# Kernel optimization log

Measured on AMD Instinct MI355X. Metric: run time of the kernel, lower is better.

The kernel has to match this reference:

```python
import jax, jax.numpy as jnp
import numpy as np

KERNEL_MUL = 2.0
KERNEL_NUM = 5


def _mmd(source, target):
    n = source.shape[0]
    m = target.shape[0]
    total = jnp.concatenate([source, target], axis=0)  # [n+m, d]
    sq = jnp.sum(total * total, axis=1)  # [n+m]
    l2 = sq[:, None] + sq[None, :] - 2.0 * (total @ total.T)  # [n+m, n+m]
    l2 = jnp.maximum(l2, 0.0)
    n_samples = n + m
    bandwidth = jnp.sum(l2) / (n_samples * n_samples - n_samples)
    bandwidth = bandwidth / (KERNEL_MUL ** (KERNEL_NUM // 2))
    # sum of KERNEL_NUM Gaussian kernels with geometric bandwidths
    kernels = sum(jnp.exp(-l2 / (bandwidth * KERNEL_MUL ** i)) for i in range(KERNEL_NUM))
    b = n  # batch_size = n, as in the torch code
    xx = jnp.sum(kernels[:b, :b]) / (n * n)
    yy = jnp.sum(kernels[b:, b:]) / (m * m)
    xy = jnp.sum(kernels[:b, b:]) / (n * m)
    yx = jnp.sum(kernels[b:, :b]) / (m * n)
    return xx + yy - xy - yx


def setup_inputs() -> dict:
    key = jax.random.key(0)
    k1, k2 = jax.random.split(key)
    source = jax.random.normal(k1, (4096, 256), dtype=jnp.float32)
    target = jax.random.normal(k2, (4096, 256), dtype=jnp.float32)
    return {"source": source, "target": target}


def reference(source, target):
    return _mmd(source, target)
```

## Files before the change

### kernel.cpp

```cpp
#include <hip/hip_runtime.h>
#include <hip/hip_bf16.h>

#define WS_D_COLSUM8 0
#define WS_D_SQSUM8  2048
#define WS_D_NEGG    2056
#define WS_D_SLOT    2057
#define WS_SLOTS     64
#define WS_MEMSET_B  16968
#define WS_SQ_OFF    17152
#define WS_G_OFF     50176

#define NROW 8192
#define HALF 4096
#define DIM  256
#define TILE 128
#define NB   64
#define NBLK (NB * (NB + 1) / 2)
#define KC   32
#define NC   (DIM / KC)
#define BUFE (TILE * KC)

typedef short  short8 __attribute__((ext_vector_type(8)));
typedef float  f32x4  __attribute__((ext_vector_type(4)));
typedef float  f32x2  __attribute__((ext_vector_type(2)));
typedef unsigned short us4 __attribute__((ext_vector_type(4)));

static __device__ __forceinline__ unsigned short f2bfbits(float f) {
    __hip_bfloat16 h = __float2bfloat16(f);
    return *reinterpret_cast<unsigned short*>(&h);
}
static __device__ __forceinline__ float bfbits2f(unsigned short u) {
    return __uint_as_float(((unsigned int)u) << 16);
}
static __device__ __forceinline__ void gl_lds16(const void* g, void* l) {
    __builtin_amdgcn_global_load_lds(
        (const __attribute__((address_space(1))) void*)g,
        (__attribute__((address_space(3))) void*)l, 16, 0, 0);
}

__global__ __launch_bounds__(256) void k_prep(const float* __restrict__ src,
                                              const float* __restrict__ tgt,
                                              unsigned short* __restrict__ G,
                                              float* __restrict__ sq,
                                              double* __restrict__ wsd) {
    __shared__ float cs_lds[4 * 256];
    __shared__ double sq_lds[4];

    int t = threadIdx.x, wid = t >> 6, lane = t & 63;
    int r0 = blockIdx.x * 16;
    int c4 = lane * 4;
    int bank = blockIdx.x & 7;

    float cs0 = 0.f, cs1 = 0.f, cs2 = 0.f, cs3 = 0.f;
    double wsq = 0.0;
    for (int i = 0; i < 4; ++i) {
        int row = r0 + wid + i * 4;
        const float* base = (row < HALF) ? (src + (size_t)row * DIM)
                                         : (tgt + (size_t)(row - HALF) * DIM);
        float4 v = *(const float4*)(base + c4);
        unsigned short u0 = f2bfbits(v.x), u1 = f2bfbits(v.y),
                       u2 = f2bfbits(v.z), u3 = f2bfbits(v.w);
        us4 uu = {u0, u1, u2, u3};
        *(us4*)(G + (size_t)row * DIM + c4) = uu;
        float r0f = bfbits2f(u0), r1f = bfbits2f(u1),
              r2f = bfbits2f(u2), r3f = bfbits2f(u3);
        cs0 += r0f; cs1 += r1f; cs2 += r2f; cs3 += r3f;
        float s = r0f * r0f + r1f * r1f + r2f * r2f + r3f * r3f;
        #pragma unroll
        for (int off = 32; off; off >>= 1) s += __shfl_down(s, off);
        if (lane == 0) { sq[row] = s; wsq += (double)s; }
    }
    cs_lds[wid * 256 + c4 + 0] = cs0;
    cs_lds[wid * 256 + c4 + 1] = cs1;
    cs_lds[wid * 256 + c4 + 2] = cs2;
    cs_lds[wid * 256 + c4 + 3] = cs3;
    if (lane == 0) sq_lds[wid] = wsq;
    __syncthreads();
    double s = (double)cs_lds[t] + (double)cs_lds[256 + t] +
               (double)cs_lds[512 + t] + (double)cs_lds[768 + t];
    atomicAdd(&wsd[WS_D_COLSUM8 + bank * 256 + t], s);
    if (t == 0)
        atomicAdd(&wsd[WS_D_SQSUM8 + bank],
                  sq_lds[0] + sq_lds[1] + sq_lds[2] + sq_lds[3]);
}

__global__ __launch_bounds__(256) void k_bw(const float* __restrict__ sq,
                                            double* __restrict__ wsd) {
    __shared__ double red[256];
    __shared__ double red2[256];
    int t = threadIdx.x;
    double s = 0.0;
    for (int i = t; i < NROW; i += 256) s += (double)sq[i];
    double c = 0.0;
    #pragma unroll
    for (int p = 0; p < 8; ++p) c += wsd[WS_D_COLSUM8 + p * 256 + t];
    red[t]  = s;
    red2[t] = c * c;
    __syncthreads();
    for (int off = 128; off; off >>= 1) {
        if (t < off) { red[t] += red[t + off]; red2[t] += red2[t + off]; }
        __syncthreads();
    }
    if (t == 0) {
        const double N = (double)NROW;
        double sum_l2 = 2.0 * N * red[0] - 2.0 * red2[0];
        double bw = sum_l2 / (N * N - N);
        bw = bw / 4.0;
        wsd[WS_D_NEGG] = -1.4426950408889634 / (16.0 * bw);
    }
}

__global__ __launch_bounds__(256, 3) void k_mmd(const unsigned short* __restrict__ G,
                                                const float* __restrict__ sq,
                                                const double* __restrict__ wsd,
                                                double* __restrict__ slots) {
    __shared__ unsigned short As[3 * BUFE];
    __shared__ unsigned short Bs[3 * BUFE];
    __shared__ double wsum[4];

    int bi = 0, rem = blockIdx.x;
    while (rem >= NB - bi) { rem -= NB - bi; ++bi; }
    int bj = bi + rem;

    int t = threadIdx.x, wid = t >> 6, lane = t & 63;
    int wr = wid >> 1, wc = wid & 1;
    int rl = lane & 15, klane = lane >> 4;

    const unsigned short* Abase = G + (size_t)bi * TILE * DIM;
    const unsigned short* Bbase = G + (size_t)bj * TILE * DIM;

    int lr0 = wid * 32 + (lane >> 2);
    int slog0 = (lane & 3) ^ ((lr0 >> 1) & 3);
    int lr1 = lr0 + 16;
    int slog1 = (lane & 3) ^ ((lr1 >> 1) & 3);
    size_t ga0 = (size_t)lr0 * DIM + slog0 * 8;
    size_t ga1 = (size_t)lr1 * DIM + slog1 * 8;
    int ld0 = (wid * 32) * KC;
    int ld1 = (wid * 32 + 16) * KC;

    int aoff[4], boff[4];
    #pragma unroll
    for (int f = 0; f < 4; ++f) {
        int ra = wr * 64 + f * 16 + rl;
        aoff[f] = ra * KC + ((klane ^ ((ra >> 1) & 3)) * 8);
        int rb = wc * 64 + f * 16 + rl;
        boff[f] = rb * KC + ((klane ^ ((rb >> 1) & 3)) * 8);
    }

    const f32x4 zero4 = {0.f, 0.f, 0.f, 0.f};
    f32x4 acc[4][4];
    #pragma unroll
    for (int i = 0; i < 4; ++i)
        #pragma unroll
        for (int j = 0; j < 4; ++j) acc[i][j] = zero4;

    #define STAGE(kc, b)                                                     \
        do {                                                                 \
            gl_lds16(Abase + ga0 + (kc) * KC, &As[(b) * BUFE + ld0]);        \
            gl_lds16(Bbase + ga0 + (kc) * KC, &Bs[(b) * BUFE + ld0]);        \
            gl_lds16(Abase + ga1 + (kc) * KC, &As[(b) * BUFE + ld1]);        \
            gl_lds16(Bbase + ga1 + (kc) * KC, &Bs[(b) * BUFE + ld1]);        \
        } while (0)

    STAGE(0, 0);
    STAGE(1, 1);

    #pragma unroll
    for (int kc = 0; kc < NC; ++kc) {
        if (kc < NC - 1) { asm volatile("s_waitcnt vmcnt(4)" ::: "memory"); }
        else             { asm volatile("s_waitcnt vmcnt(0)" ::: "memory"); }
        __builtin_amdgcn_s_barrier();
        __builtin_amdgcn_sched_barrier(0);
        if (kc + 2 < NC) STAGE(kc + 2, (kc + 2) % 3);

        const unsigned short* Ab = &As[(kc % 3) * BUFE];
        const unsigned short* Bb = &Bs[(kc % 3) * BUFE];
        short8 af[4], bfv[4];
        #pragma unroll
        for (int f = 0; f < 4; ++f) {
            af[f]  = *(const short8*)&Ab[aoff[f]];
            bfv[f] = *(const short8*)&Bb[boff[f]];
        }
        #pragma unroll
        for (int i = 0; i < 4; ++i)
            #pragma unroll
            for (int j = 0; j < 4; ++j)
                acc[i][j] = __builtin_amdgcn_mfma_f32_16x16x32_bf16(
                    af[i], bfv[j], acc[i][j], 0, 0, 0);
    }
    #undef STAGE

    int gi0 = bi * TILE + wr * 64;
    int gj0 = bj * TILE + wc * 64;
    float ng2 = (float)wsd[WS_D_NEGG];
    float m2g = -2.0f * ng2;
    f32x2 m2g2 = {m2g, m2g};
    int rgrp = lane >> 4;

    float sqb4[4];
    #pragma unroll
    for (int j = 0; j < 4; ++j) sqb4[j] = sq[gj0 + j * 16 + rl] * ng2;

    f32x2 tsv = {0.f, 0.f};
    #pragma unroll
    for (int i = 0; i < 4; ++i) {
        int base = gi0 + i * 16 + rgrp * 4;
        f32x2 sa01 = {sq[base + 0] * ng2, sq[base + 1] * ng2};
        f32x2 sa23 = {sq[base + 2] * ng2, sq[base + 3] * ng2};
        #pragma unroll
        for (int j = 0; j < 4; ++j) {
            f32x2 sb = {sqb4[j], sqb4[j]};
            f32x2 x01 = {acc[i][j][0], acc[i][j][1]};
            f32x2 x23 = {acc[i][j][2], acc[i][j][3]};
            x01 = x01 * m2g2 + (sa01 + sb);
            x23 = x23 * m2g2 + (sa23 + sb);
            f32x2 e01, e23;
            e01.x = exp2f(x01.x); e01.y = exp2f(x01.y);
            e23.x = exp2f(x23.x); e23.y = exp2f(x23.y);
            f32x2 p01 = e01 * e01, q01 = p01 * p01,
                  r01 = q01 * q01, s01 = r01 * r01;
            f32x2 p23 = e23 * e23, q23 = p23 * p23,
                  r23 = q23 * q23, s23 = r23 * r23;
            tsv += ((e01 + p01) + (q01 + r01)) + s01;
            tsv += ((e23 + p23) + (q23 + r23)) + s23;
        }
    }
    float tsum = tsv.x + tsv.y;

    float w = ((bi < 32) == (bj < 32)) ? 1.f : -1.f;
    if (bi != bj) w *= 2.f;
    double dsum = (double)tsum * (double)w;

    #pragma unroll
    for (int off = 32; off; off >>= 1) dsum += __shfl_down(dsum, off);
    if (lane == 0) wsum[wid] = dsum;
    __syncthreads();
    if (t == 0)
        atomicAdd(&slots[blockIdx.x & (WS_SLOTS - 1)],
                  wsum[0] + wsum[1] + wsum[2] + wsum[3]);
}

__global__ void k_final(const double* __restrict__ wsd, float* __restrict__ out) {
    double s = 0.0;
    for (int i = 0; i < WS_SLOTS; ++i) s += wsd[WS_D_SLOT + i];
    out[0] = (float)(s / ((double)HALF * (double)HALF));
}

extern "C" void kernel_launch(void* const* d_in, const int* in_sizes, int n_in,
                              void* d_out, int out_size, void* d_ws, size_t ws_size,
                              hipStream_t stream) {
    const float* src = (const float*)d_in[0];
    const float* tgt = (const float*)d_in[1];
    float* out = (float*)d_out;

    double* wsd       = (double*)d_ws;
    float* sq         = (float*)((char*)d_ws + WS_SQ_OFF);
    unsigned short* G = (unsigned short*)((char*)d_ws + WS_G_OFF);

    hipMemsetAsync(d_ws, 0, WS_MEMSET_B, stream);

    k_prep<<<NROW / 16, 256, 0, stream>>>(src, tgt, G, sq, wsd);
    k_bw<<<1, 256, 0, stream>>>(sq, wsd);
    k_mmd<<<NBLK, 256, 0, stream>>>(G, sq, wsd, &wsd[WS_D_SLOT]);
    k_final<<<1, 1, 0, stream>>>(wsd, out);
}
```

Baseline: 65.46 us.

## Replace atomics and memset with per-block partials and tree reductions

Removes the workspace memset and all double atomicAdds. The prep kernel now writes per-block column-sum and square-sum partials using 128 blocks of 64 rows each, and k_bw reduces those partials. Each mmd block writes its own slot, and k_final reduces the 2080 slots with a 256-thread tree instead of one serial thread. This drops a memset launch and atomic contention in exchange for fewer prep blocks and slightly more reduction work.

```diff
diff --git a/kernel.cpp b/kernel.cpp
--- a/kernel.cpp
+++ b/kernel.cpp
@@ -1,14 +1,12 @@
 #include <hip/hip_runtime.h>
 #include <hip/hip_bf16.h>
 
-#define WS_D_COLSUM8 0
-#define WS_D_SQSUM8  2048
-#define WS_D_NEGG    2056
-#define WS_D_SLOT    2057
-#define WS_SLOTS     64
-#define WS_MEMSET_B  16968
-#define WS_SQ_OFF    17152
-#define WS_G_OFF     50176
+#define WS_SLOT_OFF   0
+#define WS_NEGG_OFF   16640
+#define WS_SQPART_OFF 16648
+#define WS_CSPART_OFF 17672
+#define WS_SQ_OFF     148744
+#define WS_G_OFF      181520
 
 #define NROW 8192
 #define HALF 4096
@@ -19,6 +17,7 @@
 #define KC   32
 #define NC   (DIM / KC)
 #define BUFE (TILE * KC)
+#define PREPB 128
 
 typedef short  short8 __attribute__((ext_vector_type(8)));
 typedef float  f32x4  __attribute__((ext_vector_type(4)));
@@ -42,18 +41,18 @@
                                               const float* __restrict__ tgt,
                                               unsigned short* __restrict__ G,
                                               float* __restrict__ sq,
-                                              double* __restrict__ wsd) {
+                                              float* __restrict__ cspart,
+                                              double* __restrict__ sqpart) {
     __shared__ float cs_lds[4 * 256];
     __shared__ double sq_lds[4];
 
     int t = threadIdx.x, wid = t >> 6, lane = t & 63;
-    int r0 = blockIdx.x * 16;
+    int r0 = blockIdx.x * 64;
     int c4 = lane * 4;
-    int bank = blockIdx.x & 7;
 
     float cs0 = 0.f, cs1 = 0.f, cs2 = 0.f, cs3 = 0.f;
     double wsq = 0.0;
-    for (int i = 0; i < 4; ++i) {
+    for (int i = 0; i < 16; ++i) {
         int row = r0 + wid + i * 4;
         const float* base = (row < HALF) ? (src + (size_t)row * DIM)
                                          : (tgt + (size_t)(row - HALF) * DIM);
@@ -76,24 +75,21 @@
     cs_lds[wid * 256 + c4 + 3] = cs3;
     if (lane == 0) sq_lds[wid] = wsq;
     __syncthreads();
-    double s = (double)cs_lds[t] + (double)cs_lds[256 + t] +
-               (double)cs_lds[512 + t] + (double)cs_lds[768 + t];
-    atomicAdd(&wsd[WS_D_COLSUM8 + bank * 256 + t], s);
+    float s = cs_lds[t] + cs_lds[256 + t] + cs_lds[512 + t] + cs_lds[768 + t];
+    cspart[blockIdx.x * 256 + t] = s;
     if (t == 0)
-        atomicAdd(&wsd[WS_D_SQSUM8 + bank],
-                  sq_lds[0] + sq_lds[1] + sq_lds[2] + sq_lds[3]);
-}
-
-__global__ __launch_bounds__(256) void k_bw(const float* __restrict__ sq,
-                                            double* __restrict__ wsd) {
+        sqpart[blockIdx.x] = sq_lds[0] + sq_lds[1] + sq_lds[2] + sq_lds[3];
+}
+
+__global__ __launch_bounds__(256) void k_bw(const float* __restrict__ cspart,
+                                            const double* __restrict__ sqpart,
+                                            double* __restrict__ negg) {
     __shared__ double red[256];
     __shared__ double red2[256];
     int t = threadIdx.x;
-    double s = 0.0;
-    for (int i = t; i < NROW; i += 256) s += (double)sq[i];
     double c = 0.0;
-    #pragma unroll
-    for (int p = 0; p < 8; ++p) c += wsd[WS_D_COLSUM8 + p * 256 + t];
+    for (int b = 0; b < PREPB; ++b) c += (double)cspart[b * 256 + t];
+    double s = (t < PREPB) ? sqpart[t] : 0.0;
     red[t]  = s;
     red2[t] = c * c;
     __syncthreads();
@@ -106,13 +102,13 @@
         double sum_l2 = 2.0 * N * red[0] - 2.0 * red2[0];
         double bw = sum_l2 / (N * N - N);
         bw = bw / 4.0;
-        wsd[WS_D_NEGG] = -1.4426950408889634 / (16.0 * bw);
+        negg[0] = -1.4426950408889634 / (16.0 * bw);
     }
 }
 
 __global__ __launch_bounds__(256, 3) void k_mmd(const unsigned short* __restrict__ G,
                                                 const float* __restrict__ sq,
-                                                const double* __restrict__ wsd,
+                                                const double* __restrict__ negg,
                                                 double* __restrict__ slots) {
     __shared__ unsigned short As[3 * BUFE];
     __shared__ unsigned short Bs[3 * BUFE];
@@ -192,7 +188,7 @@
 
     int gi0 = bi * TILE + wr * 64;
     int gj0 = bj * TILE + wc * 64;
-    float ng2 = (float)wsd[WS_D_NEGG];
+    float ng2 = (float)negg[0];
     float m2g = -2.0f * ng2;
     f32x2 m2g2 = {m2g, m2g};
     int rgrp = lane >> 4;
@@ -236,14 +232,23 @@
     if (lane == 0) wsum[wid] = dsum;
     __syncthreads();
     if (t == 0)
-        atomicAdd(&slots[blockIdx.x & (WS_SLOTS - 1)],
-                  wsum[0] + wsum[1] + wsum[2] + wsum[3]);
-}
-
-__global__ void k_final(const double* __restrict__ wsd, float* __restrict__ out) {
+        slots[blockIdx.x] = wsum[0] + wsum[1] + wsum[2] + wsum[3];
+}
+
+__global__ __launch_bounds__(256) void k_final(const double* __restrict__ slots,
+                                               float* __restrict__ out) {
+    __shared__ double red[256];
+    int t = threadIdx.x;
     double s = 0.0;
-    for (int i = 0; i < WS_SLOTS; ++i) s += wsd[WS_D_SLOT + i];
-    out[0] = (float)(s / ((double)HALF * (double)HALF));
+    for (int i = t; i < NBLK; i += 256) s += slots[i];
+    red[t] = s;
+    __syncthreads();
+    for (int off = 128; off; off >>= 1) {
+        if (t < off) red[t] += red[t + off];
+        __syncthreads();
+    }
+    if (t == 0)
+        out[0] = (float)(red[0] / ((double)HALF * (double)HALF));
 }
 
 extern "C" void kernel_launch(void* const* d_in, const int* in_sizes, int n_in,
@@ -253,14 +258,15 @@
     const float* tgt = (const float*)d_in[1];
     float* out = (float*)d_out;
 
-    double* wsd       = (double*)d_ws;
-    float* sq         = (float*)((char*)d_ws + WS_SQ_OFF);
+    double* slots     = (double*)((char*)d_ws + WS_SLOT_OFF);
+    double* negg      = (double*)((char*)d_ws + WS_NEGG_OFF);
+    double* sqpart    = (double*)((char*)d_ws + WS_SQPART_OFF);
+    float*  cspart    = (float*)((char*)d_ws + WS_CSPART_OFF);
+    float*  sq        = (float*)((char*)d_ws + WS_SQ_OFF);
     unsigned short* G = (unsigned short*)((char*)d_ws + WS_G_OFF);
 
-    hipMemsetAsync(d_ws, 0, WS_MEMSET_B, stream);
-
-    k_prep<<<NROW / 16, 256, 0, stream>>>(src, tgt, G, sq, wsd);
-    k_bw<<<1, 256, 0, stream>>>(sq, wsd);
-    k_mmd<<<NBLK, 256, 0, stream>>>(G, sq, wsd, &wsd[WS_D_SLOT]);
-    k_final<<<1, 1, 0, stream>>>(wsd, out);
-}
+    k_prep<<<PREPB, 256, 0, stream>>>(src, tgt, G, sq, cspart, sqpart);
+    k_bw<<<1, 256, 0, stream>>>(cspart, sqpart, negg);
+    k_mmd<<<NBLK, 256, 0, stream>>>(G, sq, negg, slots);
+    k_final<<<1, 256, 0, stream>>>(slots, out);
+}
```

Result: no change. 65.38 us (-0.1%).
